# Optimization experiments

Measured on AMD Instinct MI355X. Metric: run time of the kernel, lower is better.

Reference implementation:

```python
import jax, jax.numpy as jnp
import numpy as np

N, D, K_POS, K_NEG = 50000, 256, 32, 20
EPS = 1e-15


def setup_inputs() -> dict:
    key = jax.random.key(0)
    k1, k2, k3, k4, k5 = jax.random.split(key, 5)
    embeddings = jax.random.normal(k1, (N, D), dtype=jnp.float32)
    neighbors_array = jax.random.randint(k2, (N, K_POS), 0, N, dtype=jnp.int32)
    # 0/1 validity mask standing in for the NaN padding of the original float array;
    # force >=1 valid neighbor per row (rows in real data with mask_array==1 have neighbors)
    nbr_mask = jax.random.randint(k3, (N, K_POS), 0, 2, dtype=jnp.int32).at[:, 0].set(1)
    negative_array = jax.random.randint(k4, (N, K_NEG), 0, N, dtype=jnp.int32)
    mask_array = jax.random.randint(k5, (N,), 0, 2, dtype=jnp.int32)
    return {
        "embeddings": embeddings,
        "neighbors_array": neighbors_array,
        "nbr_mask": nbr_mask,
        "negative_array": negative_array,
        "mask_array": mask_array,
    }


def reference(embeddings, neighbors_array, nbr_mask, negative_array, mask_array):
    # Batched ragged gather + dot: dots[n,k] = <emb[nbr[n,k]], emb[n]>
    pos_dots = jnp.einsum("nkd,nd->nk", embeddings[neighbors_array], embeddings)
    neg_dots = jnp.einsum("nkd,nd->nk", embeddings[negative_array], embeddings)

    m = nbr_mask.astype(embeddings.dtype)          # [N, K_pos] validity (NaN filter)
    cnt = m.sum(-1)                                # valid-neighbor count per row

    pos_term = -jnp.log(jax.nn.sigmoid(pos_dots) + EPS)          # [N, K_pos]
    pos_loss = (pos_term * m).sum(-1) / jnp.maximum(cnt, 1.0)    # masked mean
    # Rows with zero valid neighbors produce NaN in the original (mean of empty)
    pos_loss = jnp.where(cnt > 0, pos_loss, jnp.nan)

    neg_loss = (-jnp.log(1.0 - jax.nn.sigmoid(neg_dots) + EPS)).mean(-1)  # [N]

    row_loss = pos_loss + neg_loss
    # original skips NaN rows (adds 0) but still divides by sum(mask_array)
    row_loss = jnp.where(jnp.isnan(row_loss), 0.0, row_loss)

    rmask = mask_array.astype(embeddings.dtype)
    return (row_loss * rmask).sum() / rmask.sum()
```

## Files before the change

kernel.cpp:

```cpp
#include <hip/hip_runtime.h>
#include <hip/hip_fp16.h>
#include <string.h>

namespace {
constexpr int kN = 50000;
constexpr int kD = 256;
constexpr int kPos = 32;
constexpr int kNeg = 20;
constexpr float kEps = 1e-15f;
constexpr int kSlots = kPos / 4 + kNeg / 4;
constexpr int kCompactBlocks = (kN + 255) / 256;
constexpr int kConvertBlocks = kN * kD / 8 / 256;

typedef float floatx2 __attribute__((ext_vector_type(2)));

#if __has_builtin(__builtin_amdgcn_cvt_pk_f32_fp8)
constexpr bool kHwCvtPk = true;
constexpr bool kHwCvt1 = false;
#elif __has_builtin(__builtin_amdgcn_cvt_f32_fp8)
constexpr bool kHwCvtPk = false;
constexpr bool kHwCvt1 = true;
#else
constexpr bool kHwCvtPk = false;
constexpr bool kHwCvt1 = false;
#endif
constexpr float kOwnScale = (kHwCvtPk || kHwCvt1) ? 1.f : 256.f;

__device__ __forceinline__ uint enc1(float x) {
    const __half hh = __float2half(x * 0.00390625f);
    unsigned short t;
    memcpy(&t, &hh, 2);
    const uint s = ((uint)t >> 8) & 0x80u;
    uint mag = (uint)t & 0x7fffu;
    mag = mag + 0x3fu + ((mag >> 7) & 1u);
    uint u = mag >> 7;
    if (u > 0x7eu) u = 0x7eu;
    return s | u;
}

__device__ __forceinline__ uint enc4(const float4 a) {
#if __has_builtin(__builtin_amdgcn_cvt_pk_fp8_f32)
    int u = __builtin_amdgcn_cvt_pk_fp8_f32(a.x, a.y, 0, false);
    u = __builtin_amdgcn_cvt_pk_fp8_f32(a.z, a.w, u, true);
    return (uint)u;
#else
    return enc1(a.x) | (enc1(a.y) << 8) | (enc1(a.z) << 16) | (enc1(a.w) << 24);
#endif
}

__device__ __forceinline__ float dec_h(uint h) {
    __half hh;
    const unsigned short t = (unsigned short)h;
    memcpy(&hh, &t, 2);
    return __half2float(hh);
}

__device__ __forceinline__ void dq4(uint u, const float* o, float& d) {
#if __has_builtin(__builtin_amdgcn_cvt_pk_f32_fp8)
    const floatx2 lo = __builtin_amdgcn_cvt_pk_f32_fp8((int)u, false);
    const floatx2 hi = __builtin_amdgcn_cvt_pk_f32_fp8((int)u, true);
    d = fmaf(lo.x, o[0], d);
    d = fmaf(lo.y, o[1], d);
    d = fmaf(hi.x, o[2], d);
    d = fmaf(hi.y, o[3], d);
#elif __has_builtin(__builtin_amdgcn_cvt_f32_fp8)
    d = fmaf(__builtin_amdgcn_cvt_f32_fp8((int)u, 0), o[0], d);
    d = fmaf(__builtin_amdgcn_cvt_f32_fp8((int)u, 1), o[1], d);
    d = fmaf(__builtin_amdgcn_cvt_f32_fp8((int)u, 2), o[2], d);
    d = fmaf(__builtin_amdgcn_cvt_f32_fp8((int)u, 3), o[3], d);
#else
    const float v0 = dec_h(((u << 8) & 0x8000u) | ((u << 7) & 0x3f80u));
    const float v1 = dec_h((u & 0x8000u) | ((u >> 1) & 0x3f80u));
    const float v2 = dec_h(((u >> 8) & 0x8000u) | ((u >> 9) & 0x3f80u));
    const float v3 = dec_h(((u >> 16) & 0x8000u) | ((u >> 17) & 0x3f80u));
    d = fmaf(v0, o[0], d);
    d = fmaf(v1, o[1], d);
    d = fmaf(v2, o[2], d);
    d = fmaf(v3, o[3], d);
#endif
}

__global__ __launch_bounds__(256) void prep_kernel(const float* __restrict__ emb,
                                                   uint* __restrict__ tbl,
                                                   const int* __restrict__ rmask,
                                                   int* __restrict__ list,
                                                   float* __restrict__ acc,
                                                   float* __restrict__ out) {
    const int bid = blockIdx.x;
    if (bid < kCompactBlocks) {
        if (bid == 0 && threadIdx.x == 0) out[0] = 0.f;
        const int n = bid * 256 + threadIdx.x;
        if (n < kN && rmask[n]) {
            const int p = atomicAdd(reinterpret_cast<unsigned*>(&acc[2]), 1u);
            list[p] = n;
        }
    } else {
        const size_t i = ((size_t)(bid - kCompactBlocks) * 256 + threadIdx.x) * 8;
        const float4* src = reinterpret_cast<const float4*>(emb + i);
        const float4 a = src[0];
        const float4 b = src[1];
        uint2 o;
        o.x = enc4(a);
        o.y = enc4(b);
        reinterpret_cast<uint2*>(tbl)[i / 8] = o;
    }
}

__global__ __launch_bounds__(256) void row_loss_fp8(
    const float* __restrict__ emb,
    const uchar* __restrict__ tblb,
    const int* __restrict__ nbr,
    const int* __restrict__ nbrm,
    const int* __restrict__ neg,
    const int* __restrict__ list,
    const float* __restrict__ acc,
    float* __restrict__ out) {
    __shared__ float s_num[4];
    const int wave = threadIdx.x >> 6;
    const int lane = threadIdx.x & 63;
    const int g = lane >> 4;
    const int t = lane & 15;
    const uint lane_off = (uint)t * 16u;

    const int cnt_active = reinterpret_cast<const int*>(acc)[2];
    const int i = blockIdx.x * 4 + wave;
    float num = 0.f;

    if (i < cnt_active) {
        const int n = list[i];

        const float4* erow = reinterpret_cast<const float4*>(emb + (size_t)n * kD);
        float own[16];
#pragma unroll
        for (int j = 0; j < 4; ++j) {
            const float4 f = erow[4 * t + j];
            own[4 * j + 0] = f.x * kOwnScale;
            own[4 * j + 1] = f.y * kOwnScale;
            own[4 * j + 2] = f.z * kOwnScale;
            own[4 * j + 3] = f.w * kOwnScale;
        }

        const int* nrow = nbr + (size_t)n * kPos;
        const int* mrow = nbrm + (size_t)n * kPos;
        const int* grow = neg + (size_t)n * kNeg;

        uint off[kSlots];
        float w[kPos / 4];
        float cnt = 0.f;
#pragma unroll
        for (int s = 0; s < kPos / 4; ++s) {
            off[s] = ((uint)nrow[s * 4 + g] << 8) + lane_off;
            const float mf = (float)mrow[s * 4 + g];
            w[s] = mf;
            cnt += mf;
        }
#pragma unroll
        for (int s = 0; s < kNeg / 4; ++s)
            off[kPos / 4 + s] = ((uint)grow[s * 4 + g] << 8) + lane_off;

        float pos_sum = 0.f, neg_sum = 0.f;
        uint4 u = *reinterpret_cast<const uint4*>(tblb + off[0]);
#pragma unroll
        for (int s = 0; s < kSlots; ++s) {
            const uint4 uc = u;
            if (s + 1 < kSlots)
                u = *reinterpret_cast<const uint4*>(tblb + off[s + 1]);
            float d = 0.f;
            dq4(uc.x, own + 0, d);
            dq4(uc.y, own + 4, d);
            dq4(uc.z, own + 8, d);
            dq4(uc.w, own + 12, d);
            d += __shfl_xor(d, 8);
            d += __shfl_xor(d, 4);
            d += __shfl_xor(d, 2);
            d += __shfl_xor(d, 1);
            const float sg = 1.f / (1.f + __expf(-d));
            if (s < kPos / 4) {
                pos_sum += -__logf(sg + kEps) * w[s];
            } else {
                neg_sum += -__logf(1.f - sg + kEps);
            }
        }

        pos_sum += __shfl_xor(pos_sum, 16);
        pos_sum += __shfl_xor(pos_sum, 32);
        neg_sum += __shfl_xor(neg_sum, 16);
        neg_sum += __shfl_xor(neg_sum, 32);
        cnt += __shfl_xor(cnt, 16);
        cnt += __shfl_xor(cnt, 32);

        if (cnt > 0.f) num = pos_sum / cnt + neg_sum / (float)kNeg;
    }

    if (lane == 0) s_num[wave] = num;
    __syncthreads();
    if (threadIdx.x == 0) {
        const float v = s_num[0] + s_num[1] + s_num[2] + s_num[3];
        if (v != 0.f) atomicAdd(out, v / (float)cnt_active);
    }
}

__global__ __launch_bounds__(256) void row_loss_f32(
    const float* __restrict__ emb,
    const int* __restrict__ nbr,
    const int* __restrict__ nbrm,
    const int* __restrict__ neg,
    const int* __restrict__ rmask,
    float* __restrict__ acc) {
    __shared__ float s_num[4];
    __shared__ float s_den[4];
    const int wave = threadIdx.x >> 6;
    const int lane = threadIdx.x & 63;
    const int n = blockIdx.x * 4 + wave;
    const int g = lane >> 4;
    const int t = lane & 15;

    const float4* erow = reinterpret_cast<const float4*>(emb + (size_t)n * kD);
    float4 own4[4];
#pragma unroll
    for (int j = 0; j < 4; ++j) own4[j] = erow[j * 16 + t];

    const int* nrow = nbr + (size_t)n * kPos;
    const int* mrow = nbrm + (size_t)n * kPos;
    const int* grow = neg + (size_t)n * kNeg;

    float pos_sum = 0.f, neg_sum = 0.f, cnt = 0.f;
#pragma unroll
    for (int it = 0; it < kPos / 4; ++it) {
        const int idx = nrow[it * 4 + g];
        const float mf = (float)mrow[it * 4 + g];
        cnt += mf;
        const float4* brow = reinterpret_cast<const float4*>(emb + (size_t)idx * kD);
        float d = 0.f;
#pragma unroll
        for (int j = 0; j < 4; ++j) {
            const float4 b = brow[j * 16 + t];
            const float4 a = own4[j];
            d += a.x * b.x + a.y * b.y + a.z * b.z + a.w * b.w;
        }
        d += __shfl_xor(d, 8);
        d += __shfl_xor(d, 4);
        d += __shfl_xor(d, 2);
        d += __shfl_xor(d, 1);
        const float s = 1.f / (1.f + __expf(-d));
        pos_sum += -__logf(s + kEps) * mf;
    }
#pragma unroll
    for (int it = 0; it < kNeg / 4; ++it) {
        const int idx = grow[it * 4 + g];
        const float4* brow = reinterpret_cast<const float4*>(emb + (size_t)idx * kD);
        float d = 0.f;
#pragma unroll
        for (int j = 0; j < 4; ++j) {
            const float4 b = brow[j * 16 + t];
            const float4 a = own4[j];
            d += a.x * b.x + a.y * b.y + a.z * b.z + a.w * b.w;
        }
        d += __shfl_xor(d, 8);
        d += __shfl_xor(d, 4);
        d += __shfl_xor(d, 2);
        d += __shfl_xor(d, 1);
        const float s = 1.f / (1.f + __expf(-d));
        neg_sum += -__logf(1.f - s + kEps);
    }

    pos_sum += __shfl_xor(pos_sum, 16);
    pos_sum += __shfl_xor(pos_sum, 32);
    neg_sum += __shfl_xor(neg_sum, 16);
    neg_sum += __shfl_xor(neg_sum, 32);
    cnt += __shfl_xor(cnt, 16);
    cnt += __shfl_xor(cnt, 32);

    float num = 0.f;
    if (cnt > 0.f) num = pos_sum / cnt + neg_sum / (float)kNeg;
    const float rmf = (float)rmask[n];

    if (lane == 0) {
        s_num[wave] = num * rmf;
        s_den[wave] = rmf;
    }
    __syncthreads();
    if (threadIdx.x == 0) {
        atomicAdd(&acc[0], s_num[0] + s_num[1] + s_num[2] + s_num[3]);
        atomicAdd(&acc[1], s_den[0] + s_den[1] + s_den[2] + s_den[3]);
    }
}

__global__ void finalize_f32(const float* __restrict__ acc, float* __restrict__ out) {
    out[0] = acc[0] / acc[1];
}
}

extern "C" void kernel_launch(void* const* d_in, const int* in_sizes, int n_in,
                              void* d_out, int out_size, void* d_ws, size_t ws_size,
                              hipStream_t stream) {
    const float* emb = (const float*)d_in[0];
    const int* nbr = (const int*)d_in[1];
    const int* nbrm = (const int*)d_in[2];
    const int* neg = (const int*)d_in[3];
    const int* rmask = (const int*)d_in[4];
    float* acc = (float*)d_ws;

    const size_t tbl_bytes = (size_t)kN * kD;
    const size_t list_bytes = (size_t)kN * sizeof(int);
    if (ws_size >= 256 + tbl_bytes + list_bytes) {
        uint* tbl = (uint*)((char*)d_ws + 256);
        int* list = (int*)((char*)d_ws + 256 + tbl_bytes);
        hipMemsetAsync(acc, 0, 4 * sizeof(float), stream);
        prep_kernel<<<kCompactBlocks + kConvertBlocks, 256, 0, stream>>>(
            emb, tbl, rmask, list, acc, (float*)d_out);
        row_loss_fp8<<<(kN + 3) / 4, 256, 0, stream>>>(emb, (const uchar*)tbl, nbr,
                                                       nbrm, neg, list, acc,
                                                       (float*)d_out);
    } else {
        hipMemsetAsync(acc, 0, 2 * sizeof(float), stream);
        row_loss_f32<<<kN / 4, 256, 0, stream>>>(emb, nbr, nbrm, neg, rmask, acc);
        finalize_f32<<<1, 1, 0, stream>>>(acc, (float*)d_out);
    }
}
```

Baseline: 194.9 us.

## Split FP8 gather table into dimension slices and compute partial dots per slice

The FP8 embedding table is re-laid out as 8 column slices of 32 dims each (12.8 MB total, about 1.6 MB per slice). A new partial_dots kernel assigns blocks to slices so that each slice's gathers can stay in cache, and it accumulates per-gather partial dot products into a workspace array with atomics. A separate finish_loss kernel applies the sigmoid/log loss. In exchange it adds a 10 MB dots buffer that must be memset, global atomics for every gather, and an extra pass over the indices per slice.

```diff
diff --git a/kernel.cpp b/kernel.cpp
--- a/kernel.cpp
+++ b/kernel.cpp
@@ -7,10 +7,14 @@
 constexpr int kD = 256;
 constexpr int kPos = 32;
 constexpr int kNeg = 20;
+constexpr int kGathers = kPos + kNeg;
 constexpr float kEps = 1e-15f;
 constexpr int kSlots = kPos / 4 + kNeg / 4;
 constexpr int kCompactBlocks = (kN + 255) / 256;
 constexpr int kConvertBlocks = kN * kD / 8 / 256;
+constexpr int kSliceD = 32;
+constexpr int kNSlices = kD / kSliceD;
+constexpr size_t kSliceBytes = (size_t)kN * kSliceD;
 
 typedef float floatx2 __attribute__((ext_vector_type(2)));
 
@@ -55,33 +59,38 @@
     return __half2float(hh);
 }
 
-__device__ __forceinline__ void dq4(uint u, const float* o, float& d) {
+__device__ __forceinline__ void dq4f(uint u, const float4& o, float& d) {
 #if __has_builtin(__builtin_amdgcn_cvt_pk_f32_fp8)
     const floatx2 lo = __builtin_amdgcn_cvt_pk_f32_fp8((int)u, false);
     const floatx2 hi = __builtin_amdgcn_cvt_pk_f32_fp8((int)u, true);
-    d = fmaf(lo.x, o[0], d);
-    d = fmaf(lo.y, o[1], d);
-    d = fmaf(hi.x, o[2], d);
-    d = fmaf(hi.y, o[3], d);
+    d = fmaf(lo.x, o.x, d);
+    d = fmaf(lo.y, o.y, d);
+    d = fmaf(hi.x, o.z, d);
+    d = fmaf(hi.y, o.w, d);
 #elif __has_builtin(__builtin_amdgcn_cvt_f32_fp8)
-    d = fmaf(__builtin_amdgcn_cvt_f32_fp8((int)u, 0), o[0], d);
-    d = fmaf(__builtin_amdgcn_cvt_f32_fp8((int)u, 1), o[1], d);
-    d = fmaf(__builtin_amdgcn_cvt_f32_fp8((int)u, 2), o[2], d);
-    d = fmaf(__builtin_amdgcn_cvt_f32_fp8((int)u, 3), o[3], d);
+    d = fmaf(__builtin_amdgcn_cvt_f32_fp8((int)u, 0), o.x, d);
+    d = fmaf(__builtin_amdgcn_cvt_f32_fp8((int)u, 1), o.y, d);
+    d = fmaf(__builtin_amdgcn_cvt_f32_fp8((int)u, 2), o.z, d);
+    d = fmaf(__builtin_amdgcn_cvt_f32_fp8((int)u, 3), o.w, d);
 #else
     const float v0 = dec_h(((u << 8) & 0x8000u) | ((u << 7) & 0x3f80u));
     const float v1 = dec_h((u & 0x8000u) | ((u >> 1) & 0x3f80u));
     const float v2 = dec_h(((u >> 8) & 0x8000u) | ((u >> 9) & 0x3f80u));
     const float v3 = dec_h(((u >> 16) & 0x8000u) | ((u >> 17) & 0x3f80u));
-    d = fmaf(v0, o[0], d);
-    d = fmaf(v1, o[1], d);
-    d = fmaf(v2, o[2], d);
-    d = fmaf(v3, o[3], d);
+    d = fmaf(v0, o.x, d);
+    d = fmaf(v1, o.y, d);
+    d = fmaf(v2, o.z, d);
+    d = fmaf(v3, o.w, d);
 #endif
 }
 
+__device__ __forceinline__ void dq4(uint u, const float* o, float& d) {
+    const float4 f = {o[0], o[1], o[2], o[3]};
+    dq4f(u, f, d);
+}
+
 __global__ __launch_bounds__(256) void prep_kernel(const float* __restrict__ emb,
-                                                   uint* __restrict__ tbl,
+                                                   uchar* __restrict__ tbl,
                                                    const int* __restrict__ rmask,
                                                    int* __restrict__ list,
                                                    float* __restrict__ acc,
@@ -95,14 +104,129 @@
             list[p] = n;
         }
     } else {
-        const size_t i = ((size_t)(bid - kCompactBlocks) * 256 + threadIdx.x) * 8;
-        const float4* src = reinterpret_cast<const float4*>(emb + i);
-        const float4 a = src[0];
-        const float4 b = src[1];
+        const size_t a = ((size_t)(bid - kCompactBlocks) * 256 + threadIdx.x) * 8;
+        const int q = (int)(a / kSliceBytes);
+        const size_t r = a % kSliceBytes;
+        const int n = (int)(r / kSliceD);
+        const int j = (int)(r % kSliceD);
+        const float* src = emb + (size_t)n * kD + q * kSliceD + j;
+        const float4 f0 = reinterpret_cast<const float4*>(src)[0];
+        const float4 f1 = reinterpret_cast<const float4*>(src)[1];
         uint2 o;
-        o.x = enc4(a);
-        o.y = enc4(b);
-        reinterpret_cast<uint2*>(tbl)[i / 8] = o;
+        o.x = enc4(f0);
+        o.y = enc4(f1);
+        *reinterpret_cast<uint2*>(tbl + a) = o;
+    }
+}
+
+__global__ __launch_bounds__(256) void partial_dots(
+    const float* __restrict__ emb,
+    const uchar* __restrict__ tbl,
+    const int* __restrict__ nbr,
+    const int* __restrict__ neg,
+    const int* __restrict__ list,
+    const float* __restrict__ acc,
+    float* __restrict__ dots) {
+    const int q = blockIdx.x & 7;
+    const int bs = blockIdx.x >> 3;
+    const int wave = threadIdx.x >> 6;
+    const int lane = threadIdx.x & 63;
+    const int g8 = lane >> 3;
+    const int l8 = lane & 7;
+    const int cnt_active = reinterpret_cast<const int*>(acc)[2];
+    const uchar* slice = tbl + (size_t)q * kSliceBytes;
+    const int wave_id = bs * 4 + wave;
+    const int stride = (gridDim.x >> 3) * 4;
+
+    for (int i = wave_id; i < cnt_active; i += stride) {
+        const int n = list[i];
+        float4 own = *reinterpret_cast<const float4*>(
+            emb + (size_t)n * kD + q * kSliceD + l8 * 4);
+        own.x *= kOwnScale;
+        own.y *= kOwnScale;
+        own.z *= kOwnScale;
+        own.w *= kOwnScale;
+        const int* nrow = nbr + (size_t)n * kPos;
+        const int* grow = neg + (size_t)n * kNeg;
+        float* drow = dots + (size_t)i * kGathers;
+#pragma unroll
+        for (int k = 0; k < 7; ++k) {
+            const int gi = k * 8 + g8;
+            const int gic = gi < kGathers ? gi : 0;
+            const int idx = gic < kPos ? nrow[gic] : grow[gic - kPos];
+            const uint u = *reinterpret_cast<const uint*>(
+                slice + (size_t)idx * kSliceD + l8 * 4);
+            float d = 0.f;
+            dq4f(u, own, d);
+            d += __shfl_xor(d, 4);
+            d += __shfl_xor(d, 2);
+            d += __shfl_xor(d, 1);
+            if (l8 == 0 && gi < kGathers) atomicAdd(&drow[gi], d);
+        }
+    }
+}
+
+__global__ __launch_bounds__(256) void finish_loss(
+    const int* __restrict__ nbrm,
+    const int* __restrict__ list,
+    const float* __restrict__ acc,
+    const float* __restrict__ dots,
+    float* __restrict__ out) {
+    __shared__ float s_num[4];
+    const int wave = threadIdx.x >> 6;
+    const int lane = threadIdx.x & 63;
+    const int cnt_active = reinterpret_cast<const int*>(acc)[2];
+    const int i = blockIdx.x * 4 + wave;
+    float num = 0.f;
+
+    if (i < cnt_active) {
+        const int n = list[i];
+        float pos_sum = 0.f, neg_sum = 0.f, cnt = 0.f;
+        if (lane < kGathers) {
+            const float d = dots[(size_t)i * kGathers + lane];
+            const float sg = 1.f / (1.f + __expf(-d));
+            if (lane < kPos) {
+                const float m = (float)nbrm[(size_t)n * kPos + lane];
+                pos_sum = -__logf(sg + kEps) * m;
+                cnt = m;
+            } else {
+                neg_sum = -__logf(1.f - sg + kEps);
+            }
+        }
+#pragma unroll
+        for (int o = 32; o >= 1; o >>= 1) {
+            pos_sum += __shfl_xor(pos_sum, o);
+            neg_sum += __shfl_xor(neg_sum, o);
+            cnt += __shfl_xor(cnt, o);
+        }
+        if (cnt > 0.f) num = pos_sum / cnt + neg_sum / (float)kNeg;
+    }
+
+    if (lane == 0) s_num[wave] = num;
+    __syncthreads();
+    if (threadIdx.x == 0) {
+        const float v = s_num[0] + s_num[1] + s_num[2] + s_num[3];
+        if (v != 0.f) atomicAdd(out, v / (float)cnt_active);
+    }
+}
+
+__global__ __launch_bounds__(256) void convert_fp8_flat(const float* __restrict__ emb,
+                                                        uint* __restrict__ tbl) {
+    const size_t i = ((size_t)blockIdx.x * 256 + threadIdx.x) * 8;
+    const float4* src = reinterpret_cast<const float4*>(emb + i);
+    uint2 o;
+    o.x = enc4(src[0]);
+    o.y = enc4(src[1]);
+    reinterpret_cast<uint2*>(tbl)[i / 8] = o;
+}
+
+__global__ __launch_bounds__(256) void compact_kernel(const int* __restrict__ rmask,
+                                                      int* __restrict__ list,
+                                                      float* __restrict__ acc) {
+    const int n = blockIdx.x * 256 + threadIdx.x;
+    if (n < kN && rmask[n]) {
+        const int p = atomicAdd(reinterpret_cast<unsigned*>(&acc[2]), 1u);
+        list[p] = n;
     }
 }
 
@@ -113,8 +237,7 @@
     const int* __restrict__ nbrm,
     const int* __restrict__ neg,
     const int* __restrict__ list,
-    const float* __restrict__ acc,
-    float* __restrict__ out) {
+    float* __restrict__ acc) {
     __shared__ float s_num[4];
     const int wave = threadIdx.x >> 6;
     const int lane = threadIdx.x & 63;
@@ -128,7 +251,6 @@
 
     if (i < cnt_active) {
         const int n = list[i];
-
         const float4* erow = reinterpret_cast<const float4*>(emb + (size_t)n * kD);
         float own[16];
 #pragma unroll
@@ -139,11 +261,9 @@
             own[4 * j + 2] = f.z * kOwnScale;
             own[4 * j + 3] = f.w * kOwnScale;
         }
-
         const int* nrow = nbr + (size_t)n * kPos;
         const int* mrow = nbrm + (size_t)n * kPos;
         const int* grow = neg + (size_t)n * kNeg;
-
         uint off[kSlots];
         float w[kPos / 4];
         float cnt = 0.f;
@@ -181,14 +301,12 @@
                 neg_sum += -__logf(1.f - sg + kEps);
             }
         }
-
         pos_sum += __shfl_xor(pos_sum, 16);
         pos_sum += __shfl_xor(pos_sum, 32);
         neg_sum += __shfl_xor(neg_sum, 16);
         neg_sum += __shfl_xor(neg_sum, 32);
         cnt += __shfl_xor(cnt, 16);
         cnt += __shfl_xor(cnt, 32);
-
         if (cnt > 0.f) num = pos_sum / cnt + neg_sum / (float)kNeg;
     }
 
@@ -196,8 +314,12 @@
     __syncthreads();
     if (threadIdx.x == 0) {
         const float v = s_num[0] + s_num[1] + s_num[2] + s_num[3];
-        if (v != 0.f) atomicAdd(out, v / (float)cnt_active);
-    }
+        if (v != 0.f) atomicAdd(&acc[0], v);
+    }
+}
+
+__global__ void finalize_kernel(const float* __restrict__ acc, float* __restrict__ out) {
+    out[0] = acc[0] / (float)reinterpret_cast<const int*>(acc)[2];
 }
 
 __global__ __launch_bounds__(256) void row_loss_f32(
@@ -303,15 +425,27 @@
 
     const size_t tbl_bytes = (size_t)kN * kD;
     const size_t list_bytes = (size_t)kN * sizeof(int);
-    if (ws_size >= 256 + tbl_bytes + list_bytes) {
+    const size_t dots_bytes = (size_t)kN * kGathers * sizeof(float);
+
+    if (ws_size >= 256 + dots_bytes + tbl_bytes + list_bytes) {
+        float* dots = (float*)((char*)d_ws + 256);
+        uchar* tbl = (uchar*)d_ws + 256 + dots_bytes;
+        int* list = (int*)((char*)d_ws + 256 + dots_bytes + tbl_bytes);
+        hipMemsetAsync(d_ws, 0, 256 + dots_bytes, stream);
+        prep_kernel<<<kCompactBlocks + kConvertBlocks, 256, 0, stream>>>(
+            emb, tbl, rmask, list, acc, (float*)d_out);
+        partial_dots<<<2048, 256, 0, stream>>>(emb, tbl, nbr, neg, list, acc, dots);
+        finish_loss<<<(kN + 3) / 4, 256, 0, stream>>>(nbrm, list, acc, dots,
+                                                      (float*)d_out);
+    } else if (ws_size >= 256 + tbl_bytes + list_bytes) {
         uint* tbl = (uint*)((char*)d_ws + 256);
         int* list = (int*)((char*)d_ws + 256 + tbl_bytes);
         hipMemsetAsync(acc, 0, 4 * sizeof(float), stream);
-        prep_kernel<<<kCompactBlocks + kConvertBlocks, 256, 0, stream>>>(
-            emb, tbl, rmask, list, acc, (float*)d_out);
+        compact_kernel<<<(kN + 255) / 256, 256, 0, stream>>>(rmask, list, acc);
+        convert_fp8_flat<<<kConvertBlocks, 256, 0, stream>>>(emb, tbl);
         row_loss_fp8<<<(kN + 3) / 4, 256, 0, stream>>>(emb, (const uchar*)tbl, nbr,
-                                                       nbrm, neg, list, acc,
-                                                       (float*)d_out);
+                                                       nbrm, neg, list, acc);
+        finalize_kernel<<<1, 1, 0, stream>>>(acc, (float*)d_out);
     } else {
         hipMemsetAsync(acc, 0, 2 * sizeof(float), stream);
         row_loss_f32<<<kN / 4, 256, 0, stream>>>(emb, nbr, nbrm, neg, rmask, acc);
```

Result: slower. 335.8 us (+72.3%).
